# Kernel tuning notes

Measured on AMD Instinct MI355X. Metric: run time of the kernel, lower is better.

## Reference

```python
import jax, jax.numpy as jnp
import numpy as np

B, D, T, K = 16, 256, 1024, 8192
BETA = 0.25
EPS = 1e-10


def setup_inputs() -> dict:
    key = jax.random.key(0)
    k1, k2 = jax.random.split(key)
    z = jax.random.normal(k1, (B, D, T), dtype=jnp.float32)
    # codebook initialized uniform(-1/K, 1/K) like the torch module
    embedding = jax.random.uniform(k2, (K, D), dtype=jnp.float32,
                                   minval=-1.0 / K, maxval=1.0 / K)
    return {"z": z, "embedding": embedding}


def reference(z, embedding):
    # z: [B, D, T] -> [B, T, D]
    zf = jnp.transpose(z, (0, 2, 1))
    # squared L2 distances to each codebook entry: [B, T, K]
    d = (jnp.sum(zf ** 2, axis=2, keepdims=True)
         + jnp.sum(embedding ** 2, axis=1)
         - 2.0 * jnp.einsum('btd,kd->btk', zf, embedding))
    idx = jnp.argmin(d, axis=2)                         # [B, T] int
    min_encodings = jax.nn.one_hot(idx, K, dtype=jnp.float32)  # [B, T, K]
    z_q = embedding[idx]                                # [B, T, D]
    z_q = jnp.transpose(z_q, (0, 2, 1))                 # [B, D, T]

    codebook_loss = jnp.mean((z - jax.lax.stop_gradient(z_q)) ** 2)
    commitment_loss = jnp.mean((jax.lax.stop_gradient(z) - z_q) ** 2)
    vq_loss = codebook_loss + BETA * commitment_loss

    # perplexity exactly as in torch code: mean over dim 0 only -> [T, K]
    avg_probs = jnp.mean(min_encodings, axis=0)
    perplexity = jnp.exp(-jnp.sum(avg_probs * jnp.log(avg_probs + EPS)))

    return z_q, vq_loss, perplexity, idx
```

## Files before the change

kernel.cpp:

```cpp
#include <hip/hip_runtime.h>
#include <hip/hip_bf16.h>
#include <float.h>
#include <math.h>
#include <stdint.h>

#define NB 16
#define ND 256
#define NT 1024
#define NK 8192
#define NBT (NB*NT)
#define PTS 64
#define KCH 512
#define DROWS 16
#define KHALF (NK/2)
#define NSTG ((KHALF/KCH)*(ND/DROWS))

typedef float f32x2 __attribute__((ext_vector_type(2)));
typedef const __attribute__((address_space(4))) float AS4F;


__global__ void k_ssq(const float* __restrict__ emb, float* __restrict__ ssq,
                      double* __restrict__ loss_sum, double* __restrict__ ent_sum) {
    int k = blockIdx.x * 4 + (threadIdx.x >> 6);
    int lane = threadIdx.x & 63;
    float4 v = *reinterpret_cast<const float4*>(emb + (size_t)k * ND + lane * 4);
    float s = v.x * v.x + v.y * v.y + v.z * v.z + v.w * v.w;
#pragma unroll
    for (int off = 32; off; off >>= 1) s += __shfl_down(s, off, 64);
    if (lane == 0) ssq[k] = s;
    if (blockIdx.x == 0 && threadIdx.x == 0) { *loss_sum = 0.0; *ent_sum = 0.0; }
}

__global__ __launch_bounds__(256)
void k_tr(const float* __restrict__ emb, float* __restrict__ embT) {
    __shared__ float T[64][65];
    const int kt = blockIdx.x >> 2, dt = blockIdx.x & 3;
    const int k0 = kt * 64, d0 = dt * 64;
    const int r = threadIdx.x >> 4;
    const int c4 = (threadIdx.x & 15) * 4;
#pragma unroll
    for (int j = 0; j < 4; ++j) {
        int kk = r + 16 * j;
        float4 v = *reinterpret_cast<const float4*>(emb + (size_t)(k0 + kk) * ND + d0 + c4);
        T[kk][c4 + 0] = v.x; T[kk][c4 + 1] = v.y; T[kk][c4 + 2] = v.z; T[kk][c4 + 3] = v.w;
    }
    __syncthreads();
#pragma unroll
    for (int j = 0; j < 4; ++j) {
        int dr = r + 16 * j;
        float4 w = {T[c4 + 0][dr], T[c4 + 1][dr], T[c4 + 2][dr], T[c4 + 3][dr]};
        *reinterpret_cast<float4*>(embT + (size_t)(d0 + dr) * NK + k0 + c4) = w;
    }
}

__device__ __forceinline__ void dd_fma8(f32x2 (&acc2)[8][4], float4 e0, float4 e1,
                                        float z0, float z1, float z2, float z3,
                                        float z4, float z5, float z6, float z7) {
    f32x2 e01 = {e0.x, e0.y}, e23 = {e0.z, e0.w};
    f32x2 e45 = {e1.x, e1.y}, e67 = {e1.z, e1.w};
    float zs[8] = {z0, z1, z2, z3, z4, z5, z6, z7};
#pragma unroll
    for (int p = 0; p < 8; ++p) {
        f32x2 zp2 = {zs[p], zs[p]};
        acc2[p][0] = __builtin_elementwise_fma(zp2, e01, acc2[p][0]);
        acc2[p][1] = __builtin_elementwise_fma(zp2, e23, acc2[p][1]);
        acc2[p][2] = __builtin_elementwise_fma(zp2, e45, acc2[p][2]);
        acc2[p][3] = __builtin_elementwise_fma(zp2, e67, acc2[p][3]);
    }
}

__global__ __launch_bounds__(512)
void k_main(const float* __restrict__ z, const float* __restrict__ embT,
            const float* __restrict__ ssq, float* __restrict__ pdist,
            int* __restrict__ pidx) {
    __shared__ float Es[2][DROWS][KCH];
    __shared__ float As[PTS];
    float* redD = &Es[0][0][0];
    int*   redK = reinterpret_cast<int*>(&Es[0][0][0]) + 64 * 65;

    const int tid = threadIdx.x;
    const int kh  = blockIdx.x >> 8;
    const int bid = blockIdx.x & 255;
    const int b  = bid >> 4;
    const int t0 = (bid & 15) * PTS;
    const int py = tid >> 6;
    const int kx = tid & 63;
    const int kb = kh * (KHALF / KCH);

    auto issue_stage = [&](int s, int buf) {
        const int kc2 = kb + (s >> 4), dh2 = s & 15;
        const float* gb = embT + (size_t)(dh2 * DROWS + 2 * py) * NK + kc2 * KCH + kx * 4;
#pragma unroll
        for (int j = 0; j < 2; ++j)
#pragma unroll
            for (int hf = 0; hf < 2; ++hf)
                __builtin_amdgcn_global_load_lds(
                    (const __attribute__((address_space(1))) void*)(gb + (size_t)j * NK + hf * 256),
                    (__attribute__((address_space(3))) void*)(&Es[buf][2 * py + j][hf * 256]),
                    16, 0, 0);
    };

    issue_stage(0, 0);

    if (tid < PTS) {
        const float* zp = z + ((size_t)b * ND) * NT + t0 + tid;
        float a = 0.f;
        for (int d = 0; d < ND; ++d) {
            float x = zp[(size_t)d * NT];
            a = __fadd_rn(a, __fmul_rn(x, x));
        }
        As[tid] = a;
    }

    const int wpy = __builtin_amdgcn_readfirstlane(py);
    const uint64_t zelem = ((uint64_t)b * ND) * (uint64_t)NT + (uint64_t)(t0 + wpy * 8);
    AS4F* zw = (AS4F*)(uintptr_t)(z + zelem);

    __syncthreads();

    float best[8]; int bk[8];
#pragma unroll
    for (int p = 0; p < 8; ++p) { best[p] = FLT_MAX; bk[p] = 0; }

    float zA0 = zw[0], zA1 = zw[1], zA2 = zw[2], zA3 = zw[3];
    float zA4 = zw[4], zA5 = zw[5], zA6 = zw[6], zA7 = zw[7];
    float zB0 = zw[NT + 0], zB1 = zw[NT + 1], zB2 = zw[NT + 2], zB3 = zw[NT + 3];
    float zB4 = zw[NT + 4], zB5 = zw[NT + 5], zB6 = zw[NT + 6], zB7 = zw[NT + 7];

    for (int kl = 0; kl < KHALF / KCH; ++kl) {
        const int kc = kb + kl;
        f32x2 acc2[8][4];
#pragma unroll
        for (int p = 0; p < 8; ++p)
#pragma unroll
            for (int j = 0; j < 4; ++j) acc2[p][j] = (f32x2){0.f, 0.f};

        for (int dh = 0; dh < ND / DROWS; ++dh) {
            const int s  = kl * (ND / DROWS) + dh;
            const int cb = s & 1;
            if (s + 1 < NSTG) issue_stage(s + 1, cb ^ 1);

            const float* e0b = &Es[cb][0][kx * 4];
            const float* e1b = &Es[cb][0][256 + kx * 4];
            float4 eA0 = *reinterpret_cast<const float4*>(e0b);
            float4 eA1 = *reinterpret_cast<const float4*>(e1b);
            float4 eB0 = *reinterpret_cast<const float4*>(e0b + KCH);
            float4 eB1 = *reinterpret_cast<const float4*>(e1b + KCH);
#pragma unroll
            for (int d2 = 0; d2 < DROWS / 2; ++d2) {
                dd_fma8(acc2, eA0, eA1, zA0, zA1, zA2, zA3, zA4, zA5, zA6, zA7);
                __builtin_amdgcn_sched_barrier(0);
                if (d2 + 1 < DROWS / 2) {
                    eA0 = *reinterpret_cast<const float4*>(e0b + (2 * d2 + 2) * KCH);
                    eA1 = *reinterpret_cast<const float4*>(e1b + (2 * d2 + 2) * KCH);
                }
                {
                    const size_t dnA = (size_t)((dh * DROWS + 2 * d2 + 2) & 255) * NT;
                    zA0 = zw[dnA + 0]; zA1 = zw[dnA + 1]; zA2 = zw[dnA + 2]; zA3 = zw[dnA + 3];
                    zA4 = zw[dnA + 4]; zA5 = zw[dnA + 5]; zA6 = zw[dnA + 6]; zA7 = zw[dnA + 7];
                }
                dd_fma8(acc2, eB0, eB1, zB0, zB1, zB2, zB3, zB4, zB5, zB6, zB7);
                __builtin_amdgcn_sched_barrier(0);
                if (d2 + 1 < DROWS / 2) {
                    eB0 = *reinterpret_cast<const float4*>(e0b + (2 * d2 + 3) * KCH);
                    eB1 = *reinterpret_cast<const float4*>(e1b + (2 * d2 + 3) * KCH);
                }
                {
                    const size_t dnB = (size_t)((dh * DROWS + 2 * d2 + 3) & 255) * NT;
                    zB0 = zw[dnB + 0]; zB1 = zw[dnB + 1]; zB2 = zw[dnB + 2]; zB3 = zw[dnB + 3];
                    zB4 = zw[dnB + 4]; zB5 = zw[dnB + 5]; zB6 = zw[dnB + 6]; zB7 = zw[dnB + 7];
                }
            }
            __syncthreads();
        }
        const float* sq = ssq + kc * KCH;
        float4 s0 = *reinterpret_cast<const float4*>(sq + kx * 4);
        float4 s1 = *reinterpret_cast<const float4*>(sq + 256 + kx * 4);
        float sqv[8] = {s0.x, s0.y, s0.z, s0.w, s1.x, s1.y, s1.z, s1.w};
#pragma unroll
        for (int p = 0; p < 8; ++p) {
            float A = As[py * 8 + p];
#pragma unroll
            for (int q = 0; q < 8; ++q) {
                float cq = (q & 1) ? acc2[p][q >> 1].y : acc2[p][q >> 1].x;
                float s = __fadd_rn(A, sqv[q]);
                float dist = __fsub_rn(s, 2.0f * cq);
                if (dist < best[p]) {
                    best[p] = dist;
                    bk[p] = kc * KCH + (q < 4 ? kx * 4 + q : 256 + kx * 4 + (q - 4));
                }
            }
        }
    }
    __syncthreads();
#pragma unroll
    for (int p = 0; p < 8; ++p) {
        redD[(py * 8 + p) * 65 + kx] = best[p];
        redK[(py * 8 + p) * 65 + kx] = bk[p];
    }
    __syncthreads();
    if (tid < PTS) {
        float bd = redD[tid * 65]; int bb = redK[tid * 65];
        for (int x = 1; x < 64; ++x) {
            float dx = redD[tid * 65 + x]; int kk2 = redK[tid * 65 + x];
            if (dx < bd || (dx == bd && kk2 < bb)) { bd = dx; bb = kk2; }
        }
        int pg = b * NT + t0 + tid;
        pdist[kh * NBT + pg] = bd;
        pidx [kh * NBT + pg] = bb;
    }
}

__global__ __launch_bounds__(256)
void k_red(const float* __restrict__ pdist, const int* __restrict__ pidx,
           int* __restrict__ idx_out, float* __restrict__ idxf_out) {
    int pg = blockIdx.x * 256 + threadIdx.x;
    float d0 = pdist[pg], d1 = pdist[NBT + pg];
    int   k0 = pidx[pg],  k1 = pidx[NBT + pg];
    int bb = (d1 < d0) ? k1 : k0;
    idx_out[pg] = bb;
    idxf_out[pg] = (float)bb;
}

__global__ __launch_bounds__(256)
void k_zq(const float* __restrict__ z, const float* __restrict__ emb,
          const int* __restrict__ idx, float* __restrict__ zq,
          double* __restrict__ loss_sum) {
    __shared__ int bkS[PTS];
    __shared__ double wred[4];
    const int bid = blockIdx.x;
    const int b = bid >> 4, t0 = (bid & 15) * PTS;
    const int tid = threadIdx.x;
    if (tid < PTS) bkS[tid] = idx[b * NT + t0 + tid];
    __syncthreads();
    const int i = tid & 63, dq = tid >> 6;
    const float* erow = emb + (size_t)bkS[i] * ND;
    double ls = 0.0;
    for (int j = 0; j < 64; ++j) {
        int d = dq * 64 + j;
        float qv = erow[d];
        float zv = z[((size_t)b * ND + d) * NT + t0 + i];
        float df = __fsub_rn(zv, qv);
        ls = fma((double)df, (double)df, ls);
        zq[((size_t)b * ND + d) * NT + t0 + i] = qv;
    }
#pragma unroll
    for (int off = 32; off; off >>= 1) ls += __shfl_down(ls, off, 64);
    if ((tid & 63) == 0) wred[tid >> 6] = ls;
    __syncthreads();
    if (tid == 0) atomicAdd(loss_sum, wred[0] + wred[1] + wred[2] + wred[3]);
}

__global__ void k_ent(const int* __restrict__ idx, double* __restrict__ ent_sum) {
    __shared__ double wred[4];
    int t = blockIdx.x * 256 + threadIdx.x;
    int v[16];
#pragma unroll
    for (int i = 0; i < NB; ++i) v[i] = idx[i * NT + t];
    double s = 0.0;
#pragma unroll
    for (int i = 0; i < NB; ++i) {
        bool first = true;
        for (int j = 0; j < i; ++j) if (v[j] == v[i]) first = false;
        if (first) {
            int c = 1;
            for (int j = i + 1; j < NB; ++j) c += (v[j] == v[i]);
            float p = (float)c * 0.0625f;
            s += (double)(p * logf(p + 1e-10f));
        }
    }
#pragma unroll
    for (int off = 32; off; off >>= 1) s += __shfl_down(s, off, 64);
    if ((threadIdx.x & 63) == 0) wred[threadIdx.x >> 6] = s;
    __syncthreads();
    if (threadIdx.x == 0) {
        double tot = wred[0] + wred[1] + wred[2] + wred[3];
        atomicAdd(ent_sum, tot);
    }
}

__global__ void k_fin(const double* __restrict__ loss_sum,
                      const double* __restrict__ ent_sum, float* __restrict__ out) {
    if (threadIdx.x == 0 && blockIdx.x == 0) {
        float L = (float)(*loss_sum / (double)(NB * ND * NT));
        out[4194304] = __fadd_rn(L, 0.25f * L);
        float S = (float)(-*ent_sum);
        out[4194305] = expf(fminf(S, 87.0f));
    }
}

extern "C" void kernel_launch(void* const* d_in, const int* in_sizes, int n_in,
                              void* d_out, int out_size, void* d_ws, size_t ws_size,
                              hipStream_t stream) {
    const float* z   = (const float*)d_in[0];
    const float* emb = (const float*)d_in[1];
    float* out = (float*)d_out;

    float*  ssq      = (float*)d_ws;
    int*    idx      = (int*)((char*)d_ws + 32768);
    double* loss_sum = (double*)((char*)d_ws + 98304);
    double* ent_sum  = (double*)((char*)d_ws + 98312);

    float* zq    = out;
    float* embT  = out;
    float* pdist = out + 2097152;
    int*   pidx  = (int*)(out + 2097152 + NBT * 2);
    float* idxf  = out + 4194306;

    k_ssq<<<NK / 4, 256, 0, stream>>>(emb, ssq, loss_sum, ent_sum);
    k_tr<<<(NK / 64) * (ND / 64), 256, 0, stream>>>(emb, embT);
    k_main<<<512, 512, 0, stream>>>(z, embT, ssq, pdist, pidx);
    k_red<<<NBT / 256, 256, 0, stream>>>(pdist, pidx, idx, idxf);
    k_zq<<<NBT / PTS, 256, 0, stream>>>(z, emb, idx, zq, loss_sum);
    k_ent<<<NT / 256, 256, 0, stream>>>(idx, ent_sum);
    k_fin<<<1, 64, 0, stream>>>(loss_sum, ent_sum, out);
}
```

Before: 704.4 us.

## Split codebook search four ways, shrink LDS stages, reduce argmin with wave shuffles

Splits the codebook search across four K-partitions instead of two, doubling the k_main grid to 1024 blocks. Each LDS pipeline stage now holds 8 embedding rows instead of 16, which halves the shared-memory footprint per block so more blocks can be resident per CU. The per-block argmin reduction now uses cross-lane shuffles inside each wave instead of an LDS round trip with two barriers. The trade-off is twice as many per-point partials for k_red to merge and more, shorter pipeline stages, each with its own synchronisation overhead.

```diff
diff --git a/kernel.cpp b/kernel.cpp
--- a/kernel.cpp
+++ b/kernel.cpp
@@ -11,9 +11,11 @@
 #define NBT (NB*NT)
 #define PTS 64
 #define KCH 512
-#define DROWS 16
-#define KHALF (NK/2)
-#define NSTG ((KHALF/KCH)*(ND/DROWS))
+#define DROWS 8
+#define NSPLIT 4
+#define KQ (NK/NSPLIT)
+#define DPC (ND/DROWS)
+#define NSTG ((KQ/KCH)*DPC)
 
 typedef float f32x2 __attribute__((ext_vector_type(2)));
 typedef const __attribute__((address_space(4))) float AS4F;
@@ -75,8 +77,6 @@
             int* __restrict__ pidx) {
     __shared__ float Es[2][DROWS][KCH];
     __shared__ float As[PTS];
-    float* redD = &Es[0][0][0];
-    int*   redK = reinterpret_cast<int*>(&Es[0][0][0]) + 64 * 65;
 
     const int tid = threadIdx.x;
     const int kh  = blockIdx.x >> 8;
@@ -85,19 +85,17 @@
     const int t0 = (bid & 15) * PTS;
     const int py = tid >> 6;
     const int kx = tid & 63;
-    const int kb = kh * (KHALF / KCH);
+    const int kb = kh * (KQ / KCH);
 
     auto issue_stage = [&](int s, int buf) {
-        const int kc2 = kb + (s >> 4), dh2 = s & 15;
-        const float* gb = embT + (size_t)(dh2 * DROWS + 2 * py) * NK + kc2 * KCH + kx * 4;
-#pragma unroll
-        for (int j = 0; j < 2; ++j)
-#pragma unroll
-            for (int hf = 0; hf < 2; ++hf)
-                __builtin_amdgcn_global_load_lds(
-                    (const __attribute__((address_space(1))) void*)(gb + (size_t)j * NK + hf * 256),
-                    (__attribute__((address_space(3))) void*)(&Es[buf][2 * py + j][hf * 256]),
-                    16, 0, 0);
+        const int kc2 = kb + (s >> 5), dh2 = s & 31;
+        const float* gb = embT + (size_t)(dh2 * DROWS + py) * NK + kc2 * KCH + kx * 4;
+#pragma unroll
+        for (int hf = 0; hf < 2; ++hf)
+            __builtin_amdgcn_global_load_lds(
+                (const __attribute__((address_space(1))) void*)(gb + hf * 256),
+                (__attribute__((address_space(3))) void*)(&Es[buf][py][hf * 256]),
+                16, 0, 0);
     };
 
     issue_stage(0, 0);
@@ -127,7 +125,7 @@
     float zB0 = zw[NT + 0], zB1 = zw[NT + 1], zB2 = zw[NT + 2], zB3 = zw[NT + 3];
     float zB4 = zw[NT + 4], zB5 = zw[NT + 5], zB6 = zw[NT + 6], zB7 = zw[NT + 7];
 
-    for (int kl = 0; kl < KHALF / KCH; ++kl) {
+    for (int kl = 0; kl < KQ / KCH; ++kl) {
         const int kc = kb + kl;
         f32x2 acc2[8][4];
 #pragma unroll
@@ -135,8 +133,8 @@
 #pragma unroll
             for (int j = 0; j < 4; ++j) acc2[p][j] = (f32x2){0.f, 0.f};
 
-        for (int dh = 0; dh < ND / DROWS; ++dh) {
-            const int s  = kl * (ND / DROWS) + dh;
+        for (int dh = 0; dh < DPC; ++dh) {
+            const int s  = kl * DPC + dh;
             const int cb = s & 1;
             if (s + 1 < NSTG) issue_stage(s + 1, cb ^ 1);
 
@@ -192,22 +190,20 @@
             }
         }
     }
-    __syncthreads();
 #pragma unroll
     for (int p = 0; p < 8; ++p) {
-        redD[(py * 8 + p) * 65 + kx] = best[p];
-        redK[(py * 8 + p) * 65 + kx] = bk[p];
-    }
-    __syncthreads();
-    if (tid < PTS) {
-        float bd = redD[tid * 65]; int bb = redK[tid * 65];
-        for (int x = 1; x < 64; ++x) {
-            float dx = redD[tid * 65 + x]; int kk2 = redK[tid * 65 + x];
-            if (dx < bd || (dx == bd && kk2 < bb)) { bd = dx; bb = kk2; }
-        }
-        int pg = b * NT + t0 + tid;
-        pdist[kh * NBT + pg] = bd;
-        pidx [kh * NBT + pg] = bb;
+        float bd = best[p]; int bb = bk[p];
+#pragma unroll
+        for (int off = 32; off; off >>= 1) {
+            float od = __shfl_xor(bd, off, 64);
+            int   ok = __shfl_xor(bb, off, 64);
+            if (od < bd || (od == bd && ok < bb)) { bd = od; bb = ok; }
+        }
+        if (kx == 0) {
+            int pg = b * NT + t0 + py * 8 + p;
+            pdist[kh * NBT + pg] = bd;
+            pidx [kh * NBT + pg] = bb;
+        }
     }
 }
 
@@ -215,9 +211,12 @@
 void k_red(const float* __restrict__ pdist, const int* __restrict__ pidx,
            int* __restrict__ idx_out, float* __restrict__ idxf_out) {
     int pg = blockIdx.x * 256 + threadIdx.x;
-    float d0 = pdist[pg], d1 = pdist[NBT + pg];
-    int   k0 = pidx[pg],  k1 = pidx[NBT + pg];
-    int bb = (d1 < d0) ? k1 : k0;
+    float bd = pdist[pg]; int bb = pidx[pg];
+#pragma unroll
+    for (int q = 1; q < NSPLIT; ++q) {
+        float dq = pdist[q * NBT + pg]; int kq = pidx[q * NBT + pg];
+        if (dq < bd) { bd = dq; bb = kq; }
+    }
     idx_out[pg] = bb;
     idxf_out[pg] = (float)bb;
 }
@@ -304,12 +303,12 @@
     float* zq    = out;
     float* embT  = out;
     float* pdist = out + 2097152;
-    int*   pidx  = (int*)(out + 2097152 + NBT * 2);
+    int*   pidx  = (int*)(out + 2097152 + NBT * NSPLIT);
     float* idxf  = out + 4194306;
 
     k_ssq<<<NK / 4, 256, 0, stream>>>(emb, ssq, loss_sum, ent_sum);
     k_tr<<<(NK / 64) * (ND / 64), 256, 0, stream>>>(emb, embT);
-    k_main<<<512, 512, 0, stream>>>(z, embT, ssq, pdist, pidx);
+    k_main<<<256 * NSPLIT, 512, 0, stream>>>(z, embT, ssq, pdist, pidx);
     k_red<<<NBT / 256, 256, 0, stream>>>(pdist, pidx, idx, idxf);
     k_zq<<<NBT / PTS, 256, 0, stream>>>(z, emb, idx, zq, loss_sum);
     k_ent<<<NT / 256, 256, 0, stream>>>(idx, ent_sum);
```

Result: no change. 706.7 us (+0.3%).
